# Performance work log

Hardware: AMD Instinct MI355X
Metric: run time of the kernel (lower is better)

The kernel has to match this reference:

```python
import jax, jax.numpy as jnp
import numpy as np

NEG_SLOPE = 0.2  # PyG GATConv LeakyReLU slope
N_NODES = 50000
N_EDGES = 800000
F_IN, HID, HEADS, N_CLS = 166, 64, 8, 2


def setup_inputs() -> dict:
    key = jax.random.key(0)
    ks = jax.random.split(key, 16)
    s = 0.1
    return {
        "x": jax.random.normal(ks[0], (N_NODES, F_IN), jnp.float32),
        "edge_index": jax.random.randint(ks[1], (2, N_EDGES), 0, N_NODES, jnp.int64),
        "W1": jax.random.normal(ks[2], (F_IN, HEADS * HID), jnp.float32) * s,
        "a_src1": jax.random.normal(ks[3], (HEADS, HID), jnp.float32) * s,
        "a_dst1": jax.random.normal(ks[4], (HEADS, HID), jnp.float32) * s,
        "b1": jnp.zeros((HEADS * HID,), jnp.float32),
        # conv_final: 512 -> 64, 1 head, mean (concat=False)
        "W2": jax.random.normal(ks[5], (HEADS * HID, HID), jnp.float32) * s,
        "a_src2": jax.random.normal(ks[6], (1, HID), jnp.float32) * s,
        "a_dst2": jax.random.normal(ks[7], (1, HID), jnp.float32) * s,
        "b2": jnp.zeros((HID,), jnp.float32),
        # classifier MLP 64 -> 64 -> 2
        "Wc1": jax.random.normal(ks[8], (HID, HID), jnp.float32) * s,
        "bc1": jnp.zeros((HID,), jnp.float32),
        "Wc2": jax.random.normal(ks[9], (HID, N_CLS), jnp.float32) * s,
        "bc2": jnp.zeros((N_CLS,), jnp.float32),
    }


def gat_layer(x, src, dst, W, a_src, a_dst, b, concat):
    """PyG-style GATConv (eval mode, self-loops already in src/dst)."""
    N = x.shape[0]
    H, C = a_src.shape
    xp = (x @ W).reshape(N, H, C)                 # [N,H,C] projected features
    al_src = jnp.sum(xp * a_src, axis=-1)         # [N,H]
    al_dst = jnp.sum(xp * a_dst, axis=-1)         # [N,H]
    e = jax.nn.leaky_relu(al_src[src] + al_dst[dst], NEG_SLOPE)  # [E,H]
    # segment softmax over incoming edges of each target node
    m = jax.ops.segment_max(e, dst, num_segments=N)
    ex = jnp.exp(e - m[dst])
    denom = jax.ops.segment_sum(ex, dst, num_segments=N)
    alpha = ex / denom[dst]                       # [E,H]
    out = jax.ops.segment_sum(alpha[:, :, None] * xp[src], dst, num_segments=N)  # [N,H,C]
    out = out.reshape(N, H * C) if concat else out.mean(axis=1)
    return out + b


def reference(x, edge_index, W1, a_src1, a_dst1, b1, W2, a_src2, a_dst2, b2, Wc1, bc1, Wc2, bc2):
    N = x.shape[0]
    loops = jnp.arange(N, dtype=edge_index.dtype)
    src = jnp.concatenate([edge_index[0], loops])  # add self-loops (PyG default)
    dst = jnp.concatenate([edge_index[1], loops])
    h = jax.nn.elu(gat_layer(x, src, dst, W1, a_src1, a_dst1, b1, concat=True))
    h = gat_layer(h, src, dst, W2, a_src2, a_dst2, b2, concat=False)
    h = jax.nn.relu(h @ Wc1 + bc1)
    return h @ Wc2 + bc2
```

## Files before the change

### kernel.cpp

```cpp
#include <hip/hip_runtime.h>

#define NN   50000
#define E0   800000
#define ET   850000
#define FIN  166
#define KP1  192
#define HID  64
#define NH   8
#define F1   512
#define SCHUNK 52
#define DEGPAD (1024*SCHUNK)

typedef __attribute__((ext_vector_type(8))) short short8;
typedef __attribute__((ext_vector_type(4))) float f32x4;
typedef __attribute__((ext_vector_type(4))) int int4v;
typedef unsigned short ush;

__device__ __forceinline__ float bf2f(unsigned short u){
  unsigned int x = ((unsigned int)u) << 16;
  return __builtin_bit_cast(float, x);
}
__device__ __forceinline__ unsigned short f2bf(float f){
  unsigned int x = __builtin_bit_cast(unsigned int, f);
  x += 0x7FFFu + ((x >> 16) & 1u);
  return (unsigned short)(x >> 16);
}

#define G1 (KP1/8)
#define T0V (NN*G1)
#define T1V (T0V + 512*G1)
#define T2V (T1V + 64*64)
#define T3V (T2V + ET)
__global__ __launch_bounds__(256) void k_prep_v(const float* __restrict__ x,
                                                const float* __restrict__ W1,
                                                const float* __restrict__ W2,
                                                const int* __restrict__ ei,
                                                ush* __restrict__ xpad,
                                                ush* __restrict__ W1t,
                                                ush* __restrict__ W2t,
                                                int* __restrict__ deg){
  int i = blockIdx.x*256 + threadIdx.x;
  if (i >= T3V) return;
  if (i < T0V){
    int n = i / G1, g = i - n*G1, k0 = g*8;
    short8 o;
    #pragma unroll
    for (int j = 0; j < 8; j++){
      int k = k0 + j;
      o[j] = (short)f2bf(k < FIN ? x[(size_t)n*FIN + k] : 0.f);
    }
    *(short8*)(xpad + (size_t)n*KP1 + k0) = o;
  } else if (i < T1V){
    int j = i - T0V;
    int col = j / G1, g = j - col*G1, k0 = g*8;
    short8 o;
    #pragma unroll
    for (int q = 0; q < 8; q++){
      int k = k0 + q;
      o[q] = (short)f2bf(k < FIN ? W1[(size_t)k*512 + col] : 0.f);
    }
    *(short8*)(W1t + (size_t)col*KP1 + k0) = o;
  } else if (i < T2V){
    int j = i - T1V;
    int col = j >> 6, g = j & 63, k0 = g*8;
    short8 o;
    #pragma unroll
    for (int q = 0; q < 8; q++)
      o[q] = (short)f2bf(W2[(size_t)(k0 + q)*HID + col]);
    *(short8*)(W2t + (size_t)col*F1 + k0) = o;
  } else {
    int e = i - T2V;
    int dst = (e < E0) ? ei[E0 + e] : (e - E0);
    atomicAdd(&deg[dst], 1);
  }
}

__global__ __launch_bounds__(1024) void k_scan(const int* __restrict__ deg,
                                               int* __restrict__ offs,
                                               int* __restrict__ cur){
  __shared__ int sums[1024];
  int t = threadIdx.x;
  for (int i = t; i < NN; i += 1024) cur[i] = 0;
  int base = t * SCHUNK;
  int4v v[13];
  int loc = 0;
  #pragma unroll
  for (int c = 0; c < 13; c++){
    v[c] = *(const int4v*)(deg + base + c*4);
    loc += v[c].x + v[c].y + v[c].z + v[c].w;
  }
  sums[t] = loc; __syncthreads();
  for (int off = 1; off < 1024; off <<= 1){
    int s = (t >= off) ? sums[t - off] : 0;
    __syncthreads();
    sums[t] += s;
    __syncthreads();
  }
  int run = sums[t] - loc;
  #pragma unroll
  for (int c = 0; c < 13; c++){
    int i0 = base + c*4;
    if (i0 + 0 < NN) offs[i0 + 0] = run;  run += v[c].x;
    if (i0 + 1 < NN) offs[i0 + 1] = run;  run += v[c].y;
    if (i0 + 2 < NN) offs[i0 + 2] = run;  run += v[c].z;
    if (i0 + 3 < NN) offs[i0 + 3] = run;  run += v[c].w;
  }
  if (t == 1023) offs[NN] = sums[1023];
}

__global__ __launch_bounds__(256) void k_scatter(const int* __restrict__ ei,
                                                 const int* __restrict__ offs,
                                                 int* __restrict__ cur,
                                                 int* __restrict__ esrc){
  for (int e = blockIdx.x*256 + threadIdx.x; e < ET; e += gridDim.x*256){
    int src, dst;
    if (e < E0){ src = ei[e]; dst = ei[E0 + e]; }
    else       { src = e - E0; dst = src; }
    int pos = offs[dst] + atomicAdd(&cur[dst], 1);
    esrc[pos] = src;
  }
}

__global__ __launch_bounds__(256) void k_gemm1(const ush* __restrict__ xpad,
                                               const ush* __restrict__ W1t,
                                               const float* __restrict__ a_s,
                                               const float* __restrict__ a_d,
                                               ush* __restrict__ xp1,
                                               float* __restrict__ als,
                                               float* __restrict__ ald){
  __shared__ ush As[128][40];
  __shared__ ush Bs[128][40];
  const int m0 = blockIdx.x*128, n0 = blockIdx.y*128;
  const int t = threadIdx.x, wid = t>>6, l = t&63;
  const int wr = wid>>1, wc = wid&1;
  const int lr = l&15, ksl = (l>>4)*8;
  const int srow = t>>1, sc = (t&1)*16;

  f32x4 acc[4][4];
  #pragma unroll
  for (int m = 0; m < 4; m++)
    #pragma unroll
    for (int n = 0; n < 4; n++)
      #pragma unroll
      for (int j = 0; j < 4; j++) acc[m][n][j] = 0.f;

  const int gr = m0 + srow;
  const ush* Ap = xpad + (size_t)gr*KP1 + sc;
  const ush* Bp = W1t + (size_t)(n0 + srow)*KP1 + sc;

  for (int s = 0; s < 6; s++){
    const int kk = s*32;
    short8 a0, a1;
    #pragma unroll
    for (int j = 0; j < 8; j++){ a0[j] = 0; a1[j] = 0; }
    if (gr < NN){ a0 = *(const short8*)(Ap + kk); a1 = *(const short8*)(Ap + kk + 8); }
    short8 b0 = *(const short8*)(Bp + kk);
    short8 b1 = *(const short8*)(Bp + kk + 8);
    *(short8*)&As[srow][sc]   = a0;
    *(short8*)&As[srow][sc+8] = a1;
    *(short8*)&Bs[srow][sc]   = b0;
    *(short8*)&Bs[srow][sc+8] = b1;
    __syncthreads();
    short8 af[4], bfr[4];
    #pragma unroll
    for (int m = 0; m < 4; m++) af[m]  = *(const short8*)&As[wr*64 + m*16 + lr][ksl];
    #pragma unroll
    for (int n = 0; n < 4; n++) bfr[n] = *(const short8*)&Bs[wc*64 + n*16 + lr][ksl];
    #pragma unroll
    for (int m = 0; m < 4; m++)
      #pragma unroll
      for (int n = 0; n < 4; n++)
        acc[m][n] = __builtin_amdgcn_mfma_f32_16x16x32_bf16(af[m], bfr[n], acc[m][n], 0, 0, 0);
    __syncthreads();
  }

  #pragma unroll
  for (int m = 0; m < 4; m++)
    #pragma unroll
    for (int n = 0; n < 4; n++)
      #pragma unroll
      for (int j = 0; j < 4; j++){
        int row = m0 + wr*64 + m*16 + (l>>4)*4 + j;
        int col = n0 + wc*64 + n*16 + lr;
        if (row < NN) xp1[(size_t)row*F1 + col] = f2bf(acc[m][n][j]);
      }

  const int head = blockIdx.y*2 + wc;
  float asv[4], adv[4];
  #pragma unroll
  for (int n = 0; n < 4; n++){
    asv[n] = a_s[head*64 + n*16 + lr];
    adv[n] = a_d[head*64 + n*16 + lr];
  }
  #pragma unroll
  for (int m = 0; m < 4; m++)
    #pragma unroll
    for (int j = 0; j < 4; j++){
      float ps = 0.f, pd = 0.f;
      #pragma unroll
      for (int n = 0; n < 4; n++){
        ps = fmaf(acc[m][n][j], asv[n], ps);
        pd = fmaf(acc[m][n][j], adv[n], pd);
      }
      #pragma unroll
      for (int o = 1; o < 16; o <<= 1){
        ps += __shfl_xor(ps, o, 64);
        pd += __shfl_xor(pd, o, 64);
      }
      if (lr == 0){
        int row = m0 + wr*64 + m*16 + (l>>4)*4 + j;
        if (row < NN){
          als[(size_t)row*NH + head] = fminf(fmaxf(ps, -30.f), 30.f);
          ald[(size_t)row*NH + head] = fminf(fmaxf(pd, -30.f), 30.f);
        }
      }
    }
}

__global__ __launch_bounds__(256) void k_gemm2(const ush* __restrict__ h1,
                                               const ush* __restrict__ W2t,
                                               const float* __restrict__ a_s,
                                               const float* __restrict__ a_d,
                                               ush* __restrict__ xp2,
                                               float* __restrict__ als,
                                               float* __restrict__ ald){
  __shared__ ush As[128][40];
  __shared__ ush Bs[64][40];
  const int m0 = blockIdx.x*128;
  const int t = threadIdx.x, wid = t>>6, l = t&63;
  const int lr = l&15, ksl = (l>>4)*8;
  const int srow = t>>1, sc = (t&1)*16;

  f32x4 acc[2][4];
  #pragma unroll
  for (int m = 0; m < 2; m++)
    #pragma unroll
    for (int n = 0; n < 4; n++)
      #pragma unroll
      for (int j = 0; j < 4; j++) acc[m][n][j] = 0.f;

  const int gr = m0 + srow;
  const ush* Ap = h1 + (size_t)gr*F1 + sc;
  const ush* Bp = W2t + (size_t)srow*F1 + sc;

  for (int s = 0; s < 16; s++){
    const int kk = s*32;
    short8 a0, a1;
    #pragma unroll
    for (int j = 0; j < 8; j++){ a0[j] = 0; a1[j] = 0; }
    if (gr < NN){ a0 = *(const short8*)(Ap + kk); a1 = *(const short8*)(Ap + kk + 8); }
    *(short8*)&As[srow][sc]   = a0;
    *(short8*)&As[srow][sc+8] = a1;
    if (t < 128){
      short8 b0 = *(const short8*)(Bp + kk);
      short8 b1 = *(const short8*)(Bp + kk + 8);
      *(short8*)&Bs[srow][sc]   = b0;
      *(short8*)&Bs[srow][sc+8] = b1;
    }
    __syncthreads();
    short8 af[2], bfr[4];
    #pragma unroll
    for (int m = 0; m < 2; m++) af[m]  = *(const short8*)&As[wid*32 + m*16 + lr][ksl];
    #pragma unroll
    for (int n = 0; n < 4; n++) bfr[n] = *(const short8*)&Bs[n*16 + lr][ksl];
    #pragma unroll
    for (int m = 0; m < 2; m++)
      #pragma unroll
      for (int n = 0; n < 4; n++)
        acc[m][n] = __builtin_amdgcn_mfma_f32_16x16x32_bf16(af[m], bfr[n], acc[m][n], 0, 0, 0);
    __syncthreads();
  }

  #pragma unroll
  for (int m = 0; m < 2; m++)
    #pragma unroll
    for (int n = 0; n < 4; n++)
      #pragma unroll
      for (int j = 0; j < 4; j++){
        int row = m0 + wid*32 + m*16 + (l>>4)*4 + j;
        int col = n*16 + lr;
        if (row < NN) xp2[(size_t)row*HID + col] = f2bf(acc[m][n][j]);
      }

  float asv[4], adv[4];
  #pragma unroll
  for (int n = 0; n < 4; n++){
    asv[n] = a_s[n*16 + lr];
    adv[n] = a_d[n*16 + lr];
  }
  #pragma unroll
  for (int m = 0; m < 2; m++)
    #pragma unroll
    for (int j = 0; j < 4; j++){
      float ps = 0.f, pd = 0.f;
      #pragma unroll
      for (int n = 0; n < 4; n++){
        ps = fmaf(acc[m][n][j], asv[n], ps);
        pd = fmaf(acc[m][n][j], adv[n], pd);
      }
      #pragma unroll
      for (int o = 1; o < 16; o <<= 1){
        ps += __shfl_xor(ps, o, 64);
        pd += __shfl_xor(pd, o, 64);
      }
      if (lr == 0){
        int row = m0 + wid*32 + m*16 + (l>>4)*4 + j;
        if (row < NN){
          als[row] = fminf(fmaxf(ps, -30.f), 30.f);
          ald[row] = fminf(fmaxf(pd, -30.f), 30.f);
        }
      }
    }
}

__global__ __launch_bounds__(256) void k_agg1(const int* __restrict__ offs,
                                              const int* __restrict__ esrc,
                                              const ush* __restrict__ xp1,
                                              const float* __restrict__ als,
                                              const float* __restrict__ ald,
                                              const float* __restrict__ b1,
                                              ush* __restrict__ h1){
  int w = (blockIdx.x*256 + threadIdx.x) >> 6;
  int l = threadIdx.x & 63;
  if (w >= NN) return;
  int h = l >> 3;
  int f0 = l * 8;
  float ad = ald[w*NH + h];
  int s0 = offs[w], s1 = offs[w+1];
  float accA[8], accB[8];
  #pragma unroll
  for (int j = 0; j < 8; j++){ accA[j] = 0.f; accB[j] = 0.f; }
  float den = 0.f;

  for (int base = s0; base < s1; base += 64){
    int cnt = min(64, s1 - base);
    int myE = (base + l < s1) ? esrc[base + l] : 0;
    int j = 0;
    for (; j + 4 <= cnt; j += 4){
      int sA = __shfl(myE, j,   64);
      int sB = __shfl(myE, j+1, 64);
      int sC = __shfl(myE, j+2, 64);
      int sD = __shfl(myE, j+3, 64);
      float eA = als[sA*NH + h] + ad;
      float eB = als[sB*NH + h] + ad;
      float eC = als[sC*NH + h] + ad;
      float eD = als[sD*NH + h] + ad;
      eA = fmaxf(eA, 0.2f*eA); eB = fmaxf(eB, 0.2f*eB);
      eC = fmaxf(eC, 0.2f*eC); eD = fmaxf(eD, 0.2f*eD);
      float wA = __expf(eA), wB = __expf(eB), wC = __expf(eC), wD = __expf(eD);
      short8 vA = *(const short8*)(xp1 + (size_t)sA*F1 + f0);
      short8 vB = *(const short8*)(xp1 + (size_t)sB*F1 + f0);
      short8 vC = *(const short8*)(xp1 + (size_t)sC*F1 + f0);
      short8 vD = *(const short8*)(xp1 + (size_t)sD*F1 + f0);
      den += (wA + wB) + (wC + wD);
      #pragma unroll
      for (int jj = 0; jj < 8; jj++){
        accA[jj] = fmaf(wA, bf2f((ush)vA[jj]), accA[jj]);
        accB[jj] = fmaf(wB, bf2f((ush)vB[jj]), accB[jj]);
        accA[jj] = fmaf(wC, bf2f((ush)vC[jj]), accA[jj]);
        accB[jj] = fmaf(wD, bf2f((ush)vD[jj]), accB[jj]);
      }
    }
    for (; j < cnt; j++){
      int sA = __shfl(myE, j, 64);
      float eA = als[sA*NH + h] + ad;
      eA = fmaxf(eA, 0.2f*eA);
      float wA = __expf(eA);
      short8 vA = *(const short8*)(xp1 + (size_t)sA*F1 + f0);
      den += wA;
      #pragma unroll
      for (int jj = 0; jj < 8; jj++)
        accA[jj] = fmaf(wA, bf2f((ush)vA[jj]), accA[jj]);
    }
  }
  float inv = 1.f / den;
  #pragma unroll
  for (int jj = 0; jj < 8; jj++){
    float o = (accA[jj] + accB[jj])*inv + b1[f0 + jj];
    o = o > 0.f ? o : expm1f(o);
    h1[(size_t)w*F1 + f0 + jj] = f2bf(o);
  }
}

__global__ __launch_bounds__(256) void k_agg2(const int* __restrict__ offs,
                                              const int* __restrict__ esrc,
                                              const ush* __restrict__ xp2,
                                              const float* __restrict__ als,
                                              const float* __restrict__ ald,
                                              const float* __restrict__ b2,
                                              const float* __restrict__ Wc1,
                                              const float* __restrict__ bc1,
                                              const float* __restrict__ Wc2,
                                              const float* __restrict__ bc2,
                                              float* __restrict__ out){
  int w = (blockIdx.x*256 + threadIdx.x) >> 6;
  int l = threadIdx.x & 63;
  if (w >= NN) return;
  float ad = ald[w];
  int s0 = offs[w], s1 = offs[w+1];
  float accA = 0.f, accB = 0.f, den = 0.f;

  for (int base = s0; base < s1; base += 64){
    int cnt = min(64, s1 - base);
    bool ok = (base + l < s1);
    int myE = ok ? esrc[base + l] : 0;
    float myW = 0.f;
    if (ok){
      float e_ = als[myE] + ad;
      e_ = fmaxf(e_, 0.2f*e_);
      myW = __expf(e_);
    }
    int j = 0;
    for (; j + 8 <= cnt; j += 8){
      int sA = __shfl(myE, j,   64), sB = __shfl(myE, j+1, 64);
      int sC = __shfl(myE, j+2, 64), sD = __shfl(myE, j+3, 64);
      int sE = __shfl(myE, j+4, 64), sF = __shfl(myE, j+5, 64);
      int sG = __shfl(myE, j+6, 64), sH = __shfl(myE, j+7, 64);
      float wA = __shfl(myW, j,   64), wB = __shfl(myW, j+1, 64);
      float wC = __shfl(myW, j+2, 64), wD = __shfl(myW, j+3, 64);
      float wE = __shfl(myW, j+4, 64), wF = __shfl(myW, j+5, 64);
      float wG = __shfl(myW, j+6, 64), wH = __shfl(myW, j+7, 64);
      float xA = bf2f(xp2[(size_t)sA*HID + l]);
      float xB = bf2f(xp2[(size_t)sB*HID + l]);
      float xC = bf2f(xp2[(size_t)sC*HID + l]);
      float xD = bf2f(xp2[(size_t)sD*HID + l]);
      float xE = bf2f(xp2[(size_t)sE*HID + l]);
      float xF = bf2f(xp2[(size_t)sF*HID + l]);
      float xG = bf2f(xp2[(size_t)sG*HID + l]);
      float xH = bf2f(xp2[(size_t)sH*HID + l]);
      den += ((wA + wB) + (wC + wD)) + ((wE + wF) + (wG + wH));
      accA = fmaf(wA, xA, accA); accB = fmaf(wB, xB, accB);
      accA = fmaf(wC, xC, accA); accB = fmaf(wD, xD, accB);
      accA = fmaf(wE, xE, accA); accB = fmaf(wF, xF, accB);
      accA = fmaf(wG, xG, accA); accB = fmaf(wH, xH, accB);
    }
    for (; j < cnt; j++){
      int sA = __shfl(myE, j, 64);
      float wA = __shfl(myW, j, 64);
      den += wA;
      accA = fmaf(wA, bf2f(xp2[(size_t)sA*HID + l]), accA);
    }
  }
  float h2 = (accA + accB) / den + b2[l];
  float r = 0.f;
  #pragma unroll
  for (int k = 0; k < 64; k++){
    float hk = __shfl(h2, k, 64);
    r = fmaf(hk, Wc1[k*HID + l], r);
  }
  r += bc1[l];
  r = fmaxf(r, 0.f);
  float p0 = r * Wc2[l*2 + 0];
  float p1 = r * Wc2[l*2 + 1];
  #pragma unroll
  for (int o = 1; o < 64; o <<= 1){
    p0 += __shfl_xor(p0, o, 64);
    p1 += __shfl_xor(p1, o, 64);
  }
  if (l == 0){
    out[(size_t)w*2 + 0] = p0 + bc2[0];
    out[(size_t)w*2 + 1] = p1 + bc2[1];
  }
}

extern "C" void kernel_launch(void* const* d_in, const int* in_sizes, int n_in,
                              void* d_out, int out_size, void* d_ws, size_t ws_size,
                              hipStream_t stream){
  const float* x   = (const float*)d_in[0];
  const int*   ei  = (const int*)  d_in[1];
  const float* W1  = (const float*)d_in[2];
  const float* as1 = (const float*)d_in[3];
  const float* ad1 = (const float*)d_in[4];
  const float* b1  = (const float*)d_in[5];
  const float* W2  = (const float*)d_in[6];
  const float* as2 = (const float*)d_in[7];
  const float* ad2 = (const float*)d_in[8];
  const float* b2  = (const float*)d_in[9];
  const float* Wc1 = (const float*)d_in[10];
  const float* bc1 = (const float*)d_in[11];
  const float* Wc2 = (const float*)d_in[12];
  const float* bc2 = (const float*)d_in[13];
  float* out = (float*)d_out;

  char* p = (char*)d_ws; size_t off = 0;
  auto alloc = [&](size_t b){ void* r = p + off; off = (off + b + 255) & ~(size_t)255; return r; };
  ush* xpad = (ush*)alloc((size_t)NN*KP1*2);
  ush* W1t  = (ush*)alloc((size_t)512*KP1*2);
  ush* W2t  = (ush*)alloc((size_t)HID*F1*2);
  ush* xp1  = (ush*)alloc((size_t)NN*F1*2);
  ush* h1   = (ush*)alloc((size_t)NN*F1*2);
  ush* xp2  = (ush*)alloc((size_t)NN*HID*2);
  float* als1 = (float*)alloc((size_t)NN*NH*4);
  float* ald1 = (float*)alloc((size_t)NN*NH*4);
  float* als2 = (float*)alloc((size_t)NN*4);
  float* ald2 = (float*)alloc((size_t)NN*4);
  int* deg  = (int*)alloc((size_t)DEGPAD*4);
  int* cur  = (int*)alloc((size_t)NN*4);
  int* offs = (int*)alloc((size_t)(NN+1)*4);
  int* esrc = (int*)alloc((size_t)ET*4);

  hipMemsetAsync(deg, 0, (size_t)DEGPAD*4, stream);

  k_prep_v<<<(T3V + 255)/256, 256, 0, stream>>>(x, W1, W2, ei, xpad, W1t, W2t, deg);
  k_scan<<<1, 1024, 0, stream>>>(deg, offs, cur);
  k_scatter<<<(ET + 255)/256, 256, 0, stream>>>(ei, offs, cur, esrc);

  k_gemm1<<<dim3(391, 4), 256, 0, stream>>>(xpad, W1t, as1, ad1, xp1, als1, ald1);
  k_agg1<<<12500, 256, 0, stream>>>(offs, esrc, xp1, als1, ald1, b1, h1);

  k_gemm2<<<391, 256, 0, stream>>>(h1, W2t, as2, ad2, xp2, als2, ald2);
  k_agg2<<<12500, 256, 0, stream>>>(offs, esrc, xp2, als2, ald2, b2, Wc1, bc1, Wc2, bc2, out);
}
```

Measured before the change: 400.8 us.

## Merge CSR scatter into GEMM1 launch and move classifier to MFMA kernel

The edge scatter that builds the CSR source list now runs as extra blocks inside the first GEMM launch, so the two independent stages can overlap and one launch is dropped. The classifier MLP is taken out of agg2: agg2 now writes h2 as bf16, and a new MFMA kernel computes the 64x64 layer with ReLU and the 2-class projection. Before, each wave did a 64-step shuffle loop per node. The change adds an extra launch and an h2 round trip through memory, and rounding h2 to bf16 adds some precision loss.

```diff
diff --git a/kernel.cpp b/kernel.cpp
--- a/kernel.cpp
+++ b/kernel.cpp
@@ -10,6 +10,9 @@
 #define F1   512
 #define SCHUNK 52
 #define DEGPAD (1024*SCHUNK)
+#define G1BX 391
+#define G1BLK (G1BX*4)
+#define SCB  832
 
 typedef __attribute__((ext_vector_type(8))) short short8;
 typedef __attribute__((ext_vector_type(4))) float f32x4;
@@ -30,14 +33,17 @@
 #define T0V (NN*G1)
 #define T1V (T0V + 512*G1)
 #define T2V (T1V + 64*64)
-#define T3V (T2V + ET)
+#define T2W (T2V + 512)
+#define T3V (T2W + ET)
 __global__ __launch_bounds__(256) void k_prep_v(const float* __restrict__ x,
                                                 const float* __restrict__ W1,
                                                 const float* __restrict__ W2,
+                                                const float* __restrict__ Wc1,
                                                 const int* __restrict__ ei,
                                                 ush* __restrict__ xpad,
                                                 ush* __restrict__ W1t,
                                                 ush* __restrict__ W2t,
+                                                ush* __restrict__ Wc1t,
                                                 int* __restrict__ deg){
   int i = blockIdx.x*256 + threadIdx.x;
   if (i >= T3V) return;
@@ -68,8 +74,16 @@
     for (int q = 0; q < 8; q++)
       o[q] = (short)f2bf(W2[(size_t)(k0 + q)*HID + col]);
     *(short8*)(W2t + (size_t)col*F1 + k0) = o;
+  } else if (i < T2W){
+    int j = i - T2V;
+    int col = j >> 3, k0 = (j & 7)*8;
+    short8 o;
+    #pragma unroll
+    for (int q = 0; q < 8; q++)
+      o[q] = (short)f2bf(Wc1[(size_t)(k0 + q)*HID + col]);
+    *(short8*)(Wc1t + (size_t)col*HID + k0) = o;
   } else {
-    int e = i - T2V;
+    int e = i - T2W;
     int dst = (e < E0) ? ei[E0 + e] : (e - E0);
     atomicAdd(&deg[dst], 1);
   }
@@ -108,29 +122,32 @@
   if (t == 1023) offs[NN] = sums[1023];
 }
 
-__global__ __launch_bounds__(256) void k_scatter(const int* __restrict__ ei,
-                                                 const int* __restrict__ offs,
-                                                 int* __restrict__ cur,
-                                                 int* __restrict__ esrc){
-  for (int e = blockIdx.x*256 + threadIdx.x; e < ET; e += gridDim.x*256){
-    int src, dst;
-    if (e < E0){ src = ei[e]; dst = ei[E0 + e]; }
-    else       { src = e - E0; dst = src; }
-    int pos = offs[dst] + atomicAdd(&cur[dst], 1);
-    esrc[pos] = src;
-  }
-}
-
-__global__ __launch_bounds__(256) void k_gemm1(const ush* __restrict__ xpad,
-                                               const ush* __restrict__ W1t,
-                                               const float* __restrict__ a_s,
-                                               const float* __restrict__ a_d,
-                                               ush* __restrict__ xp1,
-                                               float* __restrict__ als,
-                                               float* __restrict__ ald){
+__global__ __launch_bounds__(256) void k_sg1(const int* __restrict__ ei,
+                                             const int* __restrict__ offs,
+                                             int* __restrict__ cur,
+                                             int* __restrict__ esrc,
+                                             const ush* __restrict__ xpad,
+                                             const ush* __restrict__ W1t,
+                                             const float* __restrict__ a_s,
+                                             const float* __restrict__ a_d,
+                                             ush* __restrict__ xp1,
+                                             float* __restrict__ als,
+                                             float* __restrict__ ald){
   __shared__ ush As[128][40];
   __shared__ ush Bs[128][40];
-  const int m0 = blockIdx.x*128, n0 = blockIdx.y*128;
+  const int bid = blockIdx.x;
+  if (bid >= G1BLK){
+    int vb = bid - G1BLK;
+    for (int e = vb*256 + (int)threadIdx.x; e < ET; e += SCB*256){
+      int src, dst;
+      if (e < E0){ src = ei[e]; dst = ei[E0 + e]; }
+      else       { src = e - E0; dst = src; }
+      int pos = offs[dst] + atomicAdd(&cur[dst], 1);
+      esrc[pos] = src;
+    }
+    return;
+  }
+  const int m0 = (bid % G1BX)*128, n0 = (bid / G1BX)*128;
   const int t = threadIdx.x, wid = t>>6, l = t&63;
   const int wr = wid>>1, wc = wid&1;
   const int lr = l&15, ksl = (l>>4)*8;
@@ -185,7 +202,7 @@
         if (row < NN) xp1[(size_t)row*F1 + col] = f2bf(acc[m][n][j]);
       }
 
-  const int head = blockIdx.y*2 + wc;
+  const int head = (bid / G1BX)*2 + wc;
   float asv[4], adv[4];
   #pragma unroll
   for (int n = 0; n < 4; n++){
@@ -388,11 +405,7 @@
                                               const float* __restrict__ als,
                                               const float* __restrict__ ald,
                                               const float* __restrict__ b2,
-                                              const float* __restrict__ Wc1,
-                                              const float* __restrict__ bc1,
-                                              const float* __restrict__ Wc2,
-                                              const float* __restrict__ bc2,
-                                              float* __restrict__ out){
+                                              ush* __restrict__ h2g){
   int w = (blockIdx.x*256 + threadIdx.x) >> 6;
   int l = threadIdx.x & 63;
   if (w >= NN) return;
@@ -442,25 +455,72 @@
     }
   }
   float h2 = (accA + accB) / den + b2[l];
-  float r = 0.f;
-  #pragma unroll
-  for (int k = 0; k < 64; k++){
-    float hk = __shfl(h2, k, 64);
-    r = fmaf(hk, Wc1[k*HID + l], r);
-  }
-  r += bc1[l];
-  r = fmaxf(r, 0.f);
-  float p0 = r * Wc2[l*2 + 0];
-  float p1 = r * Wc2[l*2 + 1];
-  #pragma unroll
-  for (int o = 1; o < 64; o <<= 1){
-    p0 += __shfl_xor(p0, o, 64);
-    p1 += __shfl_xor(p1, o, 64);
-  }
-  if (l == 0){
-    out[(size_t)w*2 + 0] = p0 + bc2[0];
-    out[(size_t)w*2 + 1] = p1 + bc2[1];
-  }
+  h2g[(size_t)w*HID + l] = f2bf(h2);
+}
+
+__global__ __launch_bounds__(256) void k_cls(const ush* __restrict__ h2g,
+                                             const ush* __restrict__ Wc1t,
+                                             const float* __restrict__ bc1,
+                                             const float* __restrict__ Wc2,
+                                             const float* __restrict__ bc2,
+                                             float* __restrict__ out){
+  const int t = threadIdx.x, wid = t>>6, l = t&63;
+  const int lr = l&15, ksl = (l>>4)*8;
+  const int m0 = blockIdx.x*128 + wid*32;
+
+  f32x4 acc[2][4];
+  #pragma unroll
+  for (int m = 0; m < 2; m++)
+    #pragma unroll
+    for (int n = 0; n < 4; n++)
+      #pragma unroll
+      for (int j = 0; j < 4; j++) acc[m][n][j] = 0.f;
+
+  #pragma unroll
+  for (int ks = 0; ks < 2; ks++){
+    short8 af[2], bfr[4];
+    #pragma unroll
+    for (int m = 0; m < 2; m++){
+      int row = m0 + m*16 + lr;
+      row = row < NN ? row : NN-1;
+      af[m] = *(const short8*)(h2g + (size_t)row*HID + ks*32 + ksl);
+    }
+    #pragma unroll
+    for (int n = 0; n < 4; n++)
+      bfr[n] = *(const short8*)(Wc1t + (size_t)(n*16 + lr)*HID + ks*32 + ksl);
+    #pragma unroll
+    for (int m = 0; m < 2; m++)
+      #pragma unroll
+      for (int n = 0; n < 4; n++)
+        acc[m][n] = __builtin_amdgcn_mfma_f32_16x16x32_bf16(af[m], bfr[n], acc[m][n], 0, 0, 0);
+  }
+
+  #pragma unroll
+  for (int m = 0; m < 2; m++)
+    #pragma unroll
+    for (int j = 0; j < 4; j++){
+      float q0 = 0.f, q1 = 0.f;
+      #pragma unroll
+      for (int n = 0; n < 4; n++){
+        int col = n*16 + lr;
+        float r = acc[m][n][j] + bc1[col];
+        r = fmaxf(r, 0.f);
+        q0 = fmaf(r, Wc2[col*2 + 0], q0);
+        q1 = fmaf(r, Wc2[col*2 + 1], q1);
+      }
+      #pragma unroll
+      for (int o = 1; o < 16; o <<= 1){
+        q0 += __shfl_xor(q0, o, 64);
+        q1 += __shfl_xor(q1, o, 64);
+      }
+      if (lr == 0){
+        int row = m0 + m*16 + (l>>4)*4 + j;
+        if (row < NN){
+          out[(size_t)row*2 + 0] = q0 + bc2[0];
+          out[(size_t)row*2 + 1] = q1 + bc2[1];
+        }
+      }
+    }
 }
 
 extern "C" void kernel_launch(void* const* d_in, const int* in_sizes, int n_in,
@@ -487,9 +547,11 @@
   ush* xpad = (ush*)alloc((size_t)NN*KP1*2);
   ush* W1t  = (ush*)alloc((size_t)512*KP1*2);
   ush* W2t  = (ush*)alloc((size_t)HID*F1*2);
+  ush* Wc1t = (ush*)alloc((size_t)HID*HID*2);
   ush* xp1  = (ush*)alloc((size_t)NN*F1*2);
   ush* h1   = (ush*)alloc((size_t)NN*F1*2);
   ush* xp2  = (ush*)alloc((size_t)NN*HID*2);
+  ush* h2g  = (ush*)alloc((size_t)NN*HID*2);
   float* als1 = (float*)alloc((size_t)NN*NH*4);
   float* ald1 = (float*)alloc((size_t)NN*NH*4);
   float* als2 = (float*)alloc((size_t)NN*4);
@@ -501,13 +563,13 @@
 
   hipMemsetAsync(deg, 0, (size_t)DEGPAD*4, stream);
 
-  k_prep_v<<<(T3V + 255)/256, 256, 0, stream>>>(x, W1, W2, ei, xpad, W1t, W2t, deg);
+  k_prep_v<<<(T3V + 255)/256, 256, 0, stream>>>(x, W1, W2, Wc1, ei, xpad, W1t, W2t, Wc1t, deg);
   k_scan<<<1, 1024, 0, stream>>>(deg, offs, cur);
-  k_scatter<<<(ET + 255)/256, 256, 0, stream>>>(ei, offs, cur, esrc);
-
-  k_gemm1<<<dim3(391, 4), 256, 0, stream>>>(xpad, W1t, as1, ad1, xp1, als1, ald1);
+  k_sg1<<<G1BLK + SCB, 256, 0, stream>>>(ei, offs, cur, esrc,
+                                         xpad, W1t, as1, ad1, xp1, als1, ald1);
   k_agg1<<<12500, 256, 0, stream>>>(offs, esrc, xp1, als1, ald1, b1, h1);
 
   k_gemm2<<<391, 256, 0, stream>>>(h1, W2t, as2, ad2, xp2, als2, ald2);
-  k_agg2<<<12500, 256, 0, stream>>>(offs, esrc, xp2, als2, ald2, b2, Wc1, bc1, Wc2, bc2, out);
-}
+  k_agg2<<<12500, 256, 0, stream>>>(offs, esrc, xp2, als2, ald2, b2, h2g);
+  k_cls<<<391, 256, 0, stream>>>(h2g, Wc1t, bc1, Wc2, bc2, out);
+}
```

New measurement: 371.6 us. 7.3% less time.
